# Kernel optimization log

Hardware: AMD Instinct MI355X
Metric: run time of the kernel (lower is better)

## Reference

```python
import jax, jax.numpy as jnp
import numpy as np

T, B = 32, 512          # frames, batch
HALF = 42               # rows per hand (21 landmarks x 2 coords)
HF = 300                # per-hand feature size
HID = 500               # hidden size
OUT = 10                # output classes
DN = ('NCH', 'OIH', 'NCH')


def setup_inputs() -> dict:
    key = jax.random.key(0)
    ks = jax.random.split(key, 18)
    n = lambda k, s: jax.random.normal(k, s, dtype=jnp.float32) * 0.05
    return dict(
        hand_data=jax.random.normal(ks[0], (T, B, 2 * HALF), dtype=jnp.float32),
        hidden=jnp.zeros((B, HID), jnp.float32),
        l_conv_w=n(ks[1], (16, 2, 2)), l_conv_b=n(ks[2], (16,)),
        l_fc_w=n(ks[3], (HF, 304)),    l_fc_b=n(ks[4], (HF,)),
        r_conv_w=n(ks[5], (16, 2, 2)), r_conv_b=n(ks[6], (16,)),
        r_fc_w=n(ks[7], (HF, 304)),    r_fc_b=n(ks[8], (HF,)),
        conv2_w=n(ks[9], (32, 2, 2)),  conv2_b=n(ks[10], (32,)),
        l2_w=n(ks[11], (HID, 9504)),   l2_b=n(ks[12], (HID,)),
        h2h_w=n(ks[13], (HID, HID)),   h2h_b=n(ks[14], (HID,)),
        out_w=n(ks[15], (OUT, HID)),   out_b=n(ks[16], (OUT,)),
    )


def _maxpool1d(y, k):
    return jax.lax.reduce_window(y, -jnp.inf, jax.lax.max,
                                 (1, 1, k), (1, 1, 1), 'VALID')


def _hand(x, cw, cb, fw, fb):
    # x: (N, 2, 21) -> conv k2 -> (N,16,20) -> relu -> pool k2 -> (N,16,19)
    y = jax.lax.conv_general_dilated(x, cw, (1,), 'VALID', dimension_numbers=DN)
    y = jax.nn.relu(y + cb[None, :, None])
    y = _maxpool1d(y, 2)
    y = y.reshape(y.shape[0], -1)          # (N, 304)
    return jax.nn.relu(y @ fw.T + fb)      # (N, 300)


def reference(hand_data, hidden,
              l_conv_w, l_conv_b, l_fc_w, l_fc_b,
              r_conv_w, r_conv_b, r_fc_w, r_fc_b,
              conv2_w, conv2_b, l2_w, l2_b,
              h2h_w, h2h_b, out_w, out_b):
    t, b, r = hand_data.shape
    half = r // 2
    # (T,B,42) -> (T*B,21,2) -> (T*B,2,21); per-frame branches have no
    # recurrence, so we vectorize them over all frames at once.
    left = jnp.swapaxes(hand_data[:, :, :half].reshape(t * b, -1, 2), 1, 2)
    right = jnp.swapaxes(hand_data[:, :, half:].reshape(t * b, -1, 2), 1, 2)
    lo = _hand(left, l_conv_w, l_conv_b, l_fc_w, l_fc_b)    # (T*B, 300)
    ro = _hand(right, r_conv_w, r_conv_b, r_fc_w, r_fc_b)   # (T*B, 300)
    both = jnp.stack([lo, ro], axis=1)                       # (T*B, 2, 300)
    y = jax.lax.conv_general_dilated(both, conv2_w, (1,), 'VALID',
                                     dimension_numbers=DN)   # (T*B, 32, 299)
    y = jax.nn.relu(y + conv2_b[None, :, None])
    y = _maxpool1d(y, 3)                                     # (T*B, 32, 297)
    y = y.reshape(t * b, -1)                                 # (T*B, 9504)
    i2h = (y @ l2_w.T + l2_b).reshape(t, b, -1)              # (T, B, 500)

    def step(h, i2h_t):
        h = h @ h2h_w.T + h2h_b                              # hidden = h2h(hidden)
        out = jax.nn.relu((i2h_t + h) @ out_w.T + out_b)
        return h, out

    hidden, outs = jax.lax.scan(step, hidden, i2h)
    return outs[-1], hidden
```

## Files before the change

### kernel.cpp

```cpp
#include <hip/hip_runtime.h>
#include <hip/hip_bf16.h>


typedef __attribute__((ext_vector_type(8))) unsigned short us8;
typedef __attribute__((ext_vector_type(8))) __bf16 bf8v;
typedef __attribute__((ext_vector_type(4))) float f4v;

static __device__ __forceinline__ unsigned short f2bf(float x) {
    __hip_bfloat16 h = __float2bfloat16(x);
    return *reinterpret_cast<unsigned short*>(&h);
}

static __device__ __forceinline__ void gload16(const void* g, void* s) {
    typedef __attribute__((address_space(1))) const void gv_t;
    typedef __attribute__((address_space(3))) void sv_t;
    __builtin_amdgcn_global_load_lds((gv_t*)g, (sv_t*)s, 16, 0, 0);
}

static __device__ __forceinline__ float4 ldg4_guard(
    const float* __restrict__ p, int r, int R, int c, int C, int ld)
{
    float4 v = make_float4(0.f, 0.f, 0.f, 0.f);
    if (r < R) {
        if (c + 3 < C) {
            v = *(const float4*)(p + (size_t)r * ld + c);
        } else {
            float tmp[4] = {0.f, 0.f, 0.f, 0.f};
            for (int u = 0; u < 4; ++u)
                if (c + u < C) tmp[u] = p[(size_t)r * ld + c + u];
            v = make_float4(tmp[0], tmp[1], tmp[2], tmp[3]);
        }
    }
    return v;
}

#define KSTR 9536

__global__ __launch_bounds__(256, 2) void mfma_bt(
    const unsigned short* __restrict__ A, const unsigned short* __restrict__ B,
    float* __restrict__ Cp, int nper, int ntot)
{
    __shared__ alignas(16) unsigned short Al[2][4096];
    __shared__ alignas(16) unsigned short Bl[2][4096];
    const int bm = blockIdx.x * 64, bn = blockIdx.y * 64;
    const int z = blockIdx.z;
    int s0 = z * nper;
    int s1 = s0 + nper; if (s1 > ntot) s1 = ntot;
    const int ns = s1 - s0;
    const int t = threadIdx.x, w = t >> 6, l = t & 63;
    const int srow = l >> 3;
    const int sslot = (l & 7) ^ srow;
    const int wm = (w >> 1) * 32, wn = (w & 1) * 32;
    const int fr = l & 15, jj = l >> 4;
    f4v acc[2][2] = {};

    const unsigned short* Ab = A + (size_t)(bm + 16 * w + srow) * KSTR + sslot * 8;
    const unsigned short* Bb = B + (size_t)(bn + 16 * w + srow) * KSTR + sslot * 8;

#define STAGE(buf, st)                                                          \
    {                                                                           \
        size_t k0 = (size_t)(s0 + (st)) * 64;                                   \
        _Pragma("unroll")                                                       \
        for (int q = 0; q < 2; ++q) {                                           \
            gload16(Ab + (size_t)(8 * q) * KSTR + k0,                           \
                    &Al[buf][(16 * w + 8 * q) * 64]);                           \
            gload16(Bb + (size_t)(8 * q) * KSTR + k0,                           \
                    &Bl[buf][(16 * w + 8 * q) * 64]);                           \
        }                                                                       \
    }

#define COMPUTE(buf)                                                            \
    {                                                                           \
        _Pragma("unroll")                                                       \
        for (int kk = 0; kk < 2; ++kk) {                                        \
            bf8v af[2], bf[2];                                                  \
            _Pragma("unroll")                                                   \
            for (int f = 0; f < 2; ++f) {                                       \
                int rA = wm + f * 16 + fr;                                      \
                int pA = (jj + 4 * kk) ^ (rA & 7);                              \
                af[f] = __builtin_bit_cast(bf8v,                                \
                        *(const us8*)&Al[buf][rA * 64 + pA * 8]);               \
                int rB = wn + f * 16 + fr;                                      \
                int pB = (jj + 4 * kk) ^ (rB & 7);                              \
                bf[f] = __builtin_bit_cast(bf8v,                                \
                        *(const us8*)&Bl[buf][rB * 64 + pB * 8]);               \
            }                                                                   \
            _Pragma("unroll")                                                   \
            for (int fi = 0; fi < 2; ++fi)                                      \
                _Pragma("unroll")                                               \
                for (int fj = 0; fj < 2; ++fj)                                  \
                    acc[fi][fj] = __builtin_amdgcn_mfma_f32_16x16x32_bf16(      \
                        af[fi], bf[fj], acc[fi][fj], 0, 0, 0);                  \
        }                                                                       \
    }

    STAGE(0, 0);
    __syncthreads();
    int cur = 0;
    for (int st = 0; st < ns; ++st) {
        if (st + 1 < ns) STAGE(cur ^ 1, st + 1);
        COMPUTE(cur);
        __syncthreads();
        cur ^= 1;
    }

    float* Cz = Cp + (size_t)z * 262144;
#pragma unroll
    for (int fi = 0; fi < 2; ++fi)
#pragma unroll
        for (int fj = 0; fj < 2; ++fj)
#pragma unroll
            for (int r = 0; r < 4; ++r) {
                int m = bm + wm + fi * 16 + jj * 4 + r;
                int n = bn + wn + fj * 16 + fr;
                Cz[(size_t)m * 512 + n] = acc[fi][fj][r];
            }
#undef STAGE
#undef COMPUTE
}


__global__ __launch_bounds__(256) void fc_gemm(
    const float* __restrict__ hpL, const float* __restrict__ hpR,
    const float* __restrict__ lfw, const float* __restrict__ rfw,
    const float* __restrict__ lfb, const float* __restrict__ rfb,
    float* __restrict__ both)
{
    __shared__ alignas(16) float As[16][68];
    __shared__ alignas(16) float Bs[16][68];
    const int hand = blockIdx.z;
    const float* A = hand ? hpR : hpL;
    const float* B = hand ? rfw : lfw;
    const float* bias = hand ? rfb : lfb;
    const int t = threadIdx.x;
    const int bm = blockIdx.x * 64, bn = blockIdx.y * 64;
    const int lr = t >> 2, kq = (t & 3) * 4;
    const int ty = t >> 4, tx = t & 15;
    float acc[4][4] = {};
    float4 a0 = *(const float4*)(A + (size_t)(bm + lr) * 304 + kq);
    float4 b0 = (bn + lr < 300)
        ? *(const float4*)(B + (size_t)(bn + lr) * 304 + kq)
        : make_float4(0.f, 0.f, 0.f, 0.f);
    for (int ks = 0; ks < 19; ++ks) {
        __syncthreads();
        As[kq + 0][lr] = a0.x; As[kq + 1][lr] = a0.y;
        As[kq + 2][lr] = a0.z; As[kq + 3][lr] = a0.w;
        Bs[kq + 0][lr] = b0.x; Bs[kq + 1][lr] = b0.y;
        Bs[kq + 2][lr] = b0.z; Bs[kq + 3][lr] = b0.w;
        __syncthreads();
        if (ks < 18) {
            int kb = (ks + 1) * 16 + kq;
            a0 = *(const float4*)(A + (size_t)(bm + lr) * 304 + kb);
            b0 = (bn + lr < 300)
                ? *(const float4*)(B + (size_t)(bn + lr) * 304 + kb)
                : make_float4(0.f, 0.f, 0.f, 0.f);
        }
#pragma unroll
        for (int k = 0; k < 16; ++k) {
            float4 av = *(const float4*)&As[k][ty * 4];
            float4 bv = *(const float4*)&Bs[k][tx * 4];
            float aa[4] = {av.x, av.y, av.z, av.w};
            float bb[4] = {bv.x, bv.y, bv.z, bv.w};
#pragma unroll
            for (int i = 0; i < 4; ++i)
#pragma unroll
                for (int j = 0; j < 4; ++j)
                    acc[i][j] = fmaf(aa[i], bb[j], acc[i][j]);
        }
    }
#pragma unroll
    for (int i = 0; i < 4; ++i) {
        int m = bm + ty * 4 + i;
#pragma unroll
        for (int j = 0; j < 4; ++j) {
            int n = bn + tx * 4 + j;
            if (n < 300)
                both[(size_t)m * 600 + hand * 300 + n] =
                    fmaxf(acc[i][j] + bias[n], 0.f);
        }
    }
}

__global__ __launch_bounds__(256) void sq_gemm(
    const float* __restrict__ P, float* __restrict__ Psum)
{
    __shared__ alignas(16) float As[16][68];
    __shared__ alignas(16) float Bs[16][68];
    const int t = threadIdx.x;
    const int bm = blockIdx.x * 64, bn = blockIdx.y * 64, z = blockIdx.z;
    const int k0 = z * 128;
    const int kend = (k0 + 128 < 500) ? k0 + 128 : 500;
    const int lr = t >> 2, kq = (t & 3) * 4;
    const int kr = t >> 4, cq = (t & 15) * 4;
    const int ty = t >> 4, tx = t & 15;
    float acc[4][4] = {};
    float4 a0 = ldg4_guard(P, bm + lr, 500, k0 + kq, kend, 500);
    float4 b0 = ldg4_guard(P, k0 + kr, kend, bn + cq, 500, 500);
    for (int ks = 0; ks < 8; ++ks) {
        __syncthreads();
        As[kq + 0][lr] = a0.x; As[kq + 1][lr] = a0.y;
        As[kq + 2][lr] = a0.z; As[kq + 3][lr] = a0.w;
        *(float4*)&Bs[kr][cq] = b0;
        __syncthreads();
        if (ks < 7) {
            a0 = ldg4_guard(P, bm + lr, 500, k0 + (ks + 1) * 16 + kq, kend, 500);
            b0 = ldg4_guard(P, k0 + (ks + 1) * 16 + kr, kend, bn + cq, 500, 500);
        }
#pragma unroll
        for (int k = 0; k < 16; ++k) {
            float4 av = *(const float4*)&As[k][ty * 4];
            float4 bv = *(const float4*)&Bs[k][tx * 4];
            float aa[4] = {av.x, av.y, av.z, av.w};
            float bb[4] = {bv.x, bv.y, bv.z, bv.w};
#pragma unroll
            for (int i = 0; i < 4; ++i)
#pragma unroll
                for (int j = 0; j < 4; ++j)
                    acc[i][j] = fmaf(aa[i], bb[j], acc[i][j]);
        }
    }
    float* Cz = Psum + (size_t)z * 250000;
#pragma unroll
    for (int i = 0; i < 4; ++i) {
        int m = bm + ty * 4 + i;
        if (m >= 500) continue;
#pragma unroll
        for (int j = 0; j < 4; ++j) {
            int n = bn + tx * 4 + j;
            if (n < 500) Cz[(size_t)m * 500 + n] = acc[i][j];
        }
    }
}

__global__ __launch_bounds__(256) void sq_red(
    const float* __restrict__ Psum, float* __restrict__ Pn,
    const float* __restrict__ u, const float* __restrict__ Pold,
    float* __restrict__ un)
{
    __shared__ float red[4];
    const int x = blockIdx.x, t = threadIdx.x;
    if (x < 977) {
        int idx = x * 256 + t;
        if (idx < 250000)
            Pn[idx] = Psum[idx] + Psum[250000 + idx] +
                      Psum[500000 + idx] + Psum[750000 + idx];
    } else {
        int j = x - 977;
        const float* row = Pold + (size_t)j * 500;
        float s = 0.f;
        for (int a = t; a < 500; a += 256) s += u[a] * row[a];
        for (int off = 32; off; off >>= 1) s += __shfl_down(s, off);
        if ((t & 63) == 0) red[t >> 6] = s;
        __syncthreads();
        if (t == 0) un[j] = red[0] + red[1] + red[2] + red[3] + u[j];
    }
}

__global__ __launch_bounds__(256) void h_gemm(
    const float* __restrict__ A, const float* __restrict__ B,
    float* __restrict__ Hsum)
{
    __shared__ alignas(16) float As[16][68];
    __shared__ alignas(16) float Bs[16][68];
    const int t = threadIdx.x;
    const int bm = blockIdx.x * 64, bn = blockIdx.y * 64, z = blockIdx.z;
    const int k0 = z * 128;
    const int kend = (k0 + 128 < 500) ? k0 + 128 : 500;
    const int lr = t >> 2, kq = (t & 3) * 4;
    const int ty = t >> 4, tx = t & 15;
    float acc[4][4] = {};
    float4 a0 = ldg4_guard(A, bm + lr, 512, k0 + kq, kend, 500);
    float4 b0 = ldg4_guard(B, bn + lr, 500, k0 + kq, kend, 500);
    for (int ks = 0; ks < 8; ++ks) {
        __syncthreads();
        As[kq + 0][lr] = a0.x; As[kq + 1][lr] = a0.y;
        As[kq + 2][lr] = a0.z; As[kq + 3][lr] = a0.w;
        Bs[kq + 0][lr] = b0.x; Bs[kq + 1][lr] = b0.y;
        Bs[kq + 2][lr] = b0.z; Bs[kq + 3][lr] = b0.w;
        __syncthreads();
        if (ks < 7) {
            a0 = ldg4_guard(A, bm + lr, 512, k0 + (ks + 1) * 16 + kq, kend, 500);
            b0 = ldg4_guard(B, bn + lr, 500, k0 + (ks + 1) * 16 + kq, kend, 500);
        }
#pragma unroll
        for (int k = 0; k < 16; ++k) {
            float4 av = *(const float4*)&As[k][ty * 4];
            float4 bv = *(const float4*)&Bs[k][tx * 4];
            float aa[4] = {av.x, av.y, av.z, av.w};
            float bb[4] = {bv.x, bv.y, bv.z, bv.w};
#pragma unroll
            for (int i = 0; i < 4; ++i)
#pragma unroll
                for (int j = 0; j < 4; ++j)
                    acc[i][j] = fmaf(aa[i], bb[j], acc[i][j]);
        }
    }
    float* Cz = Hsum + (size_t)z * 256000;
#pragma unroll
    for (int i = 0; i < 4; ++i) {
        int m = bm + ty * 4 + i;
#pragma unroll
        for (int j = 0; j < 4; ++j) {
            int n = bn + tx * 4 + j;
            if (n < 500) Cz[(size_t)m * 500 + n] = acc[i][j];
        }
    }
}

__global__ __launch_bounds__(128) void hand_conv(
    const float* __restrict__ hand,
    const float* __restrict__ lcw, const float* __restrict__ lcb,
    const float* __restrict__ rcw, const float* __restrict__ rcb,
    float* __restrict__ hpL, float* __restrict__ hpR)
{
    const int b = blockIdx.x;
    __shared__ float x[84];
    __shared__ float cw[2][64];
    __shared__ float cb[2][16];
    const int t = threadIdx.x;
    if (t < 84) x[t] = hand[(size_t)b * 84 + t];
    if (t < 64) { cw[0][t] = lcw[t]; cw[1][t] = rcw[t]; }
    if (t < 16) { cb[0][t] = lcb[t]; cb[1][t] = rcb[t]; }
    __syncthreads();
    for (int idx = t; idx < 608; idx += 128) {
        int hi = idx / 304, rem = idx % 304;
        int o = rem / 19, p = rem % 19;
        int off = hi * 42;
        const float* w = cw[hi];
        float w00 = w[o * 4], w01 = w[o * 4 + 1], w10 = w[o * 4 + 2], w11 = w[o * 4 + 3];
        float bs = cb[hi][o];
        float c0 = w00 * x[off + 2 * p] + w01 * x[off + 2 * p + 2] +
                   w10 * x[off + 2 * p + 1] + w11 * x[off + 2 * p + 3] + bs;
        float c1 = w00 * x[off + 2 * p + 2] + w01 * x[off + 2 * p + 4] +
                   w10 * x[off + 2 * p + 3] + w11 * x[off + 2 * p + 5] + bs;
        float v = fmaxf(fmaxf(c0, c1), 0.f);
        (hi ? hpR : hpL)[(size_t)b * 304 + rem] = v;
    }
}

__global__ __launch_bounds__(256) void conv2_feat(
    const float* __restrict__ both, const float* __restrict__ w2g,
    const float* __restrict__ b2g, unsigned short* __restrict__ feat)
{
    const int b = blockIdx.x, t = threadIdx.x;
    __shared__ float s[600];
    __shared__ float w2[128];
    __shared__ float b2[32];
    for (int i = t; i < 600; i += 256) s[i] = both[(size_t)b * 600 + i];
    if (t < 128) w2[t] = w2g[t];
    if (t < 32) b2[t] = b2g[t];
    __syncthreads();
    for (int idx = t; idx < 9536; idx += 256) {
        unsigned short ov = 0;
        if (idx < 9504) {
            int o = idx / 297, p = idx - o * 297;
            float w0 = w2[o * 4], w1 = w2[o * 4 + 1];
            float w2v = w2[o * 4 + 2], w3 = w2[o * 4 + 3], bb = b2[o];
            float m = -1e30f;
#pragma unroll
            for (int q = 0; q < 3; ++q) {
                float c = w0 * s[p + q] + w1 * s[p + q + 1] +
                          w2v * s[300 + p + q] + w3 * s[301 + p + q] + bb;
                m = fmaxf(m, c);
            }
            ov = f2bf(fmaxf(m, 0.f));
        }
        feat[(size_t)b * 9536 + idx] = ov;
    }
}

__global__ __launch_bounds__(256) void cvt_w(
    const float* __restrict__ W, unsigned short* __restrict__ Wb)
{
    int idx = blockIdx.x * 256 + threadIdx.x;
    int row = idx / 1192;
    int k8 = (idx - row * 1192) * 8;
    if (row >= 512) return;
    us8 o = (us8)0;
    if (row < 500 && k8 < 9504) {
        const float* p = W + (size_t)row * 9504 + k8;
        float4 v0 = *(const float4*)p;
        float4 v1 = *(const float4*)(p + 4);
        o[0] = f2bf(v0.x); o[1] = f2bf(v0.y); o[2] = f2bf(v0.z); o[3] = f2bf(v0.w);
        o[4] = f2bf(v1.x); o[5] = f2bf(v1.y); o[6] = f2bf(v1.z); o[7] = f2bf(v1.w);
    }
    *(us8*)(Wb + (size_t)row * 9536 + k8) = o;
}

__global__ __launch_bounds__(256) void out_final(
    const float* __restrict__ Cp, const float* __restrict__ l2b,
    const float* __restrict__ Hsum, const float* __restrict__ u32,
    const float* __restrict__ ow, const float* __restrict__ ob,
    float* __restrict__ out, float* __restrict__ hout)
{
    const int b = blockIdx.x, t = threadIdx.x;
    __shared__ float sj[512];
    __shared__ float red[10][4];
    for (int j = t; j < 500; j += 256) {
        float ih = l2b[j];
#pragma unroll
        for (int zz = 0; zz < 8; ++zz)
            ih += Cp[(size_t)zz * 262144 + (size_t)b * 512 + j];
        float h = u32[j];
#pragma unroll
        for (int zz = 0; zz < 4; ++zz)
            h += Hsum[(size_t)zz * 256000 + (size_t)b * 500 + j];
        hout[(size_t)b * 500 + j] = h;
        sj[j] = ih + h;
    }
    __syncthreads();
    const int w = t >> 6;
    for (int o = 0; o < 10; ++o) {
        float acc = 0.f;
        if (t < 500) acc += sj[t] * ow[o * 500 + t];
        if (t + 256 < 500) acc += sj[t + 256] * ow[o * 500 + t + 256];
        for (int off = 32; off; off >>= 1) acc += __shfl_down(acc, off);
        if ((t & 63) == 0) red[o][w] = acc;
    }
    __syncthreads();
    if (t < 10)
        out[(size_t)b * 10 + t] =
            fmaxf(red[t][0] + red[t][1] + red[t][2] + red[t][3] + ob[t], 0.f);
}

extern "C" void kernel_launch(void* const* d_in, const int* in_sizes, int n_in,
                              void* d_out, int out_size, void* d_ws, size_t ws_size,
                              hipStream_t stream) {
    const float* hand   = (const float*)d_in[0];
    const float* hidden = (const float*)d_in[1];
    const float* lcw = (const float*)d_in[2];
    const float* lcb = (const float*)d_in[3];
    const float* lfw = (const float*)d_in[4];
    const float* lfb = (const float*)d_in[5];
    const float* rcw = (const float*)d_in[6];
    const float* rcb = (const float*)d_in[7];
    const float* rfw = (const float*)d_in[8];
    const float* rfb = (const float*)d_in[9];
    const float* w2  = (const float*)d_in[10];
    const float* b2  = (const float*)d_in[11];
    const float* l2w = (const float*)d_in[12];
    const float* l2b = (const float*)d_in[13];
    const float* hw  = (const float*)d_in[14];
    const float* hb  = (const float*)d_in[15];
    const float* ow  = (const float*)d_in[16];
    const float* ob  = (const float*)d_in[17];

    char* wsb = (char*)d_ws;
    float* Cp   = (float*)wsb;
    float* hpL  = (float*)wsb;
    float* hpR  = (float*)(wsb + 622592);
    float* both = (float*)(wsb + 1245184);
    char* base1 = wsb + 8388608;
    unsigned short* featb = (unsigned short*)base1;
    unsigned short* wbf   = (unsigned short*)(base1 + 9764864);
    float* Psum = (float*)base1;
    float* Pa   = (float*)(base1 + 4000000);
    float* Pb   = (float*)(base1 + 5000000);
    float* ua   = (float*)(base1 + 6000000);
    float* ub   = (float*)(base1 + 6002000);
    float* Hsum = (float*)(base1 + 9764864);

    float* out  = (float*)d_out;
    float* hout = out + 5120;

    cvt_w<<<2384, 256, 0, stream>>>(l2w, wbf);
    hand_conv<<<512, 128, 0, stream>>>(hand + (size_t)31 * 512 * 84,
                                       lcw, lcb, rcw, rcb, hpL, hpR);
    fc_gemm<<<dim3(8, 5, 2), 256, 0, stream>>>(hpL, hpR, lfw, rfw, lfb, rfb, both);
    conv2_feat<<<512, 256, 0, stream>>>(both, w2, b2, featb);
    mfma_bt<<<dim3(8, 8, 8), 256, 0, stream>>>(featb, wbf, Cp, 19, 149);

    const float* Pcur = hw;
    const float* ucur = hb;
    float* Pn[5] = {Pa, Pb, Pa, Pb, Pa};
    float* un[5] = {ua, ub, ua, ub, ua};
    for (int i = 0; i < 5; i++) {
        sq_gemm<<<dim3(8, 8, 4), 256, 0, stream>>>(Pcur, Psum);
        sq_red<<<1477, 256, 0, stream>>>(Psum, Pn[i], ucur, Pcur, un[i]);
        Pcur = Pn[i];
        ucur = un[i];
    }
    h_gemm<<<dim3(8, 8, 4), 256, 0, stream>>>(hidden, Pcur, Hsum);
    out_final<<<512, 256, 0, stream>>>(Cp, l2b, Hsum, ucur, ow, ob, out, hout);
}
```

Before: 149.6 us.

## Fuse split-K partial reduction into repeated-squaring GEMM loads, drop reduce kernels

Removes the separate sq_red reduction kernels. Each squaring level now sums the four split-K partial products while loading its operands, and the same launch also computes the bias-vector update. This halves the number of launches in the recurrence chain and avoids writing and re-reading the reduced matrix. In exchange, every operand tile load now reads four source buffers, so redundant global reads grow. The change also flattens grid indexing, raises mfma_bt's minimum-blocks-per-CU launch bound from 2 to 4, and changes h_gemm to a 2-way K split.

```diff
diff --git a/kernel.cpp b/kernel.cpp
--- a/kernel.cpp
+++ b/kernel.cpp
@@ -34,18 +34,29 @@
     return v;
 }
 
+static __device__ __forceinline__ float4 ldg4_sum(
+    const float* __restrict__ p, int nsrc, int r, int R, int c, int C, int ld)
+{
+    float4 v = ldg4_guard(p, r, R, c, C, ld);
+    for (int s = 1; s < nsrc; ++s) {
+        float4 w = ldg4_guard(p + (size_t)s * 250000, r, R, c, C, ld);
+        v.x += w.x; v.y += w.y; v.z += w.z; v.w += w.w;
+    }
+    return v;
+}
+
 #define KSTR 9536
 
-__global__ __launch_bounds__(256, 2) void mfma_bt(
+__global__ __launch_bounds__(256, 4) void mfma_bt(
     const unsigned short* __restrict__ A, const unsigned short* __restrict__ B,
-    float* __restrict__ Cp, int nper, int ntot)
+    float* __restrict__ Cp)
 {
     __shared__ alignas(16) unsigned short Al[2][4096];
     __shared__ alignas(16) unsigned short Bl[2][4096];
-    const int bm = blockIdx.x * 64, bn = blockIdx.y * 64;
-    const int z = blockIdx.z;
-    int s0 = z * nper;
-    int s1 = s0 + nper; if (s1 > ntot) s1 = ntot;
+    const int lid = blockIdx.x;
+    const int z = lid & 7;
+    const int bm = ((lid >> 3) & 7) * 64, bn = ((lid >> 6) & 7) * 64;
+    int s0 = z * 19, s1 = s0 + 19; if (s1 > 149) s1 = 149;
     const int ns = s1 - s0;
     const int t = threadIdx.x, w = t >> 6, l = t & 63;
     const int srow = l >> 3;
@@ -54,21 +65,18 @@
     const int fr = l & 15, jj = l >> 4;
     f4v acc[2][2] = {};
 
-    const unsigned short* Ab = A + (size_t)(bm + 16 * w + srow) * KSTR + sslot * 8;
-    const unsigned short* Bb = B + (size_t)(bn + 16 * w + srow) * KSTR + sslot * 8;
+    const unsigned short* Ab = A + (size_t)(bm + 16*w + srow) * KSTR + sslot * 8;
+    const unsigned short* Bb = B + (size_t)(bn + 16*w + srow) * KSTR + sslot * 8;
 
 #define STAGE(buf, st)                                                          \
     {                                                                           \
         size_t k0 = (size_t)(s0 + (st)) * 64;                                   \
         _Pragma("unroll")                                                       \
         for (int q = 0; q < 2; ++q) {                                           \
-            gload16(Ab + (size_t)(8 * q) * KSTR + k0,                           \
-                    &Al[buf][(16 * w + 8 * q) * 64]);                           \
-            gload16(Bb + (size_t)(8 * q) * KSTR + k0,                           \
-                    &Bl[buf][(16 * w + 8 * q) * 64]);                           \
+            gload16(Ab + (size_t)(8*q) * KSTR + k0, &Al[buf][(16*w + 8*q)*64]); \
+            gload16(Bb + (size_t)(8*q) * KSTR + k0, &Bl[buf][(16*w + 8*q)*64]); \
         }                                                                       \
     }
-
 #define COMPUTE(buf)                                                            \
     {                                                                           \
         _Pragma("unroll")                                                       \
@@ -77,11 +85,11 @@
             _Pragma("unroll")                                                   \
             for (int f = 0; f < 2; ++f) {                                       \
                 int rA = wm + f * 16 + fr;                                      \
-                int pA = (jj + 4 * kk) ^ (rA & 7);                              \
+                int pA = (jj + 4*kk) ^ (rA & 7);                                \
                 af[f] = __builtin_bit_cast(bf8v,                                \
                         *(const us8*)&Al[buf][rA * 64 + pA * 8]);               \
                 int rB = wn + f * 16 + fr;                                      \
-                int pB = (jj + 4 * kk) ^ (rB & 7);                              \
+                int pB = (jj + 4*kk) ^ (rB & 7);                                \
                 bf[f] = __builtin_bit_cast(bf8v,                                \
                         *(const us8*)&Bl[buf][rB * 64 + pB * 8]);               \
             }                                                                   \
@@ -103,7 +111,6 @@
         __syncthreads();
         cur ^= 1;
     }
-
     float* Cz = Cp + (size_t)z * 262144;
 #pragma unroll
     for (int fi = 0; fi < 2; ++fi)
@@ -119,6 +126,124 @@
 #undef COMPUTE
 }
 
+__global__ __launch_bounds__(256) void sq_level(
+    const float* __restrict__ src, int nsrc, float* __restrict__ dst,
+    const float* __restrict__ u_in, float* __restrict__ u_out)
+{
+    __shared__ alignas(16) float As[16][68];
+    __shared__ alignas(16) float Bs[16][68];
+    const int lid = blockIdx.x, t = threadIdx.x;
+    if (lid >= 256) {
+        const int j = lid - 256;
+        float* red = (float*)As;
+        float s = 0.f;
+        for (int a = t; a < 500; a += 256) {
+            float p = src[(size_t)j * 500 + a];
+            for (int q = 1; q < nsrc; ++q)
+                p += src[(size_t)q * 250000 + (size_t)j * 500 + a];
+            s += u_in[a] * p;
+        }
+        for (int off = 32; off; off >>= 1) s += __shfl_down(s, off);
+        if ((t & 63) == 0) red[t >> 6] = s;
+        __syncthreads();
+        if (t == 0) u_out[j] = red[0] + red[1] + red[2] + red[3] + u_in[j];
+        return;
+    }
+    const int z = lid & 3;
+    const int bm = ((lid >> 2) & 7) * 64, bn = (lid >> 5) * 64;
+    const int k0 = z * 125, kend = k0 + 125;
+    const int lr = t >> 2, kq = (t & 3) * 4;
+    const int kr = t >> 4, cq = (t & 15) * 4;
+    const int ty = t >> 4, tx = t & 15;
+    float acc[4][4] = {};
+    float4 a0 = ldg4_sum(src, nsrc, bm + lr, 500, k0 + kq, kend, 500);
+    float4 b0 = ldg4_sum(src, nsrc, k0 + kr, kend, bn + cq, 500, 500);
+    for (int ks = 0; ks < 8; ++ks) {
+        __syncthreads();
+        As[kq+0][lr] = a0.x; As[kq+1][lr] = a0.y;
+        As[kq+2][lr] = a0.z; As[kq+3][lr] = a0.w;
+        *(float4*)&Bs[kr][cq] = b0;
+        __syncthreads();
+        if (ks < 7) {
+            a0 = ldg4_sum(src, nsrc, bm + lr, 500, k0 + (ks+1)*16 + kq, kend, 500);
+            b0 = ldg4_sum(src, nsrc, k0 + (ks+1)*16 + kr, kend, bn + cq, 500, 500);
+        }
+#pragma unroll
+        for (int k = 0; k < 16; ++k) {
+            float4 av = *(const float4*)&As[k][ty * 4];
+            float4 bv = *(const float4*)&Bs[k][tx * 4];
+            float aa[4] = {av.x, av.y, av.z, av.w};
+            float bb[4] = {bv.x, bv.y, bv.z, bv.w};
+#pragma unroll
+            for (int i = 0; i < 4; ++i)
+#pragma unroll
+                for (int j = 0; j < 4; ++j)
+                    acc[i][j] = fmaf(aa[i], bb[j], acc[i][j]);
+        }
+    }
+    float* Cz = dst + (size_t)z * 250000;
+#pragma unroll
+    for (int i = 0; i < 4; ++i) {
+        int m = bm + ty * 4 + i;
+        if (m >= 500) continue;
+#pragma unroll
+        for (int j = 0; j < 4; ++j) {
+            int n = bn + tx * 4 + j;
+            if (n < 500) Cz[(size_t)m * 500 + n] = acc[i][j];
+        }
+    }
+}
+
+__global__ __launch_bounds__(256) void h_gemm(
+    const float* __restrict__ A, const float* __restrict__ src,
+    float* __restrict__ Hsum)
+{
+    __shared__ alignas(16) float As[16][68];
+    __shared__ alignas(16) float Bs[16][68];
+    const int rid = blockIdx.x, t = threadIdx.x;
+    const int z = rid & 1;
+    const int bm = ((rid >> 1) & 7) * 64, bn = ((rid >> 4) & 7) * 64;
+    const int k0 = z * 250, kend = k0 + 250;
+    const int lr = t >> 2, kq = (t & 3) * 4;
+    const int ty = t >> 4, tx = t & 15;
+    float acc[4][4] = {};
+    float4 a0 = ldg4_guard(A, bm + lr, 512, k0 + kq, kend, 500);
+    float4 b0 = ldg4_sum(src, 4, bn + lr, 500, k0 + kq, kend, 500);
+    for (int ks = 0; ks < 16; ++ks) {
+        __syncthreads();
+        As[kq+0][lr] = a0.x; As[kq+1][lr] = a0.y;
+        As[kq+2][lr] = a0.z; As[kq+3][lr] = a0.w;
+        Bs[kq+0][lr] = b0.x; Bs[kq+1][lr] = b0.y;
+        Bs[kq+2][lr] = b0.z; Bs[kq+3][lr] = b0.w;
+        __syncthreads();
+        if (ks < 15) {
+            a0 = ldg4_guard(A, bm + lr, 512, k0 + (ks+1)*16 + kq, kend, 500);
+            b0 = ldg4_sum(src, 4, bn + lr, 500, k0 + (ks+1)*16 + kq, kend, 500);
+        }
+#pragma unroll
+        for (int k = 0; k < 16; ++k) {
+            float4 av = *(const float4*)&As[k][ty * 4];
+            float4 bv = *(const float4*)&Bs[k][tx * 4];
+            float aa[4] = {av.x, av.y, av.z, av.w};
+            float bb[4] = {bv.x, bv.y, bv.z, bv.w};
+#pragma unroll
+            for (int i = 0; i < 4; ++i)
+#pragma unroll
+                for (int j = 0; j < 4; ++j)
+                    acc[i][j] = fmaf(aa[i], bb[j], acc[i][j]);
+        }
+    }
+    float* Cz = Hsum + (size_t)z * 256000;
+#pragma unroll
+    for (int i = 0; i < 4; ++i) {
+        int m = bm + ty * 4 + i;
+#pragma unroll
+        for (int j = 0; j < 4; ++j) {
+            int n = bn + tx * 4 + j;
+            if (n < 500) Cz[(size_t)m * 500 + n] = acc[i][j];
+        }
+    }
+}
 
 __global__ __launch_bounds__(256) void fc_gemm(
     const float* __restrict__ hpL, const float* __restrict__ hpR,
@@ -143,10 +268,10 @@
         : make_float4(0.f, 0.f, 0.f, 0.f);
     for (int ks = 0; ks < 19; ++ks) {
         __syncthreads();
-        As[kq + 0][lr] = a0.x; As[kq + 1][lr] = a0.y;
-        As[kq + 2][lr] = a0.z; As[kq + 3][lr] = a0.w;
-        Bs[kq + 0][lr] = b0.x; Bs[kq + 1][lr] = b0.y;
-        Bs[kq + 2][lr] = b0.z; Bs[kq + 3][lr] = b0.w;
+        As[kq+0][lr] = a0.x; As[kq+1][lr] = a0.y;
+        As[kq+2][lr] = a0.z; As[kq+3][lr] = a0.w;
+        Bs[kq+0][lr] = b0.x; Bs[kq+1][lr] = b0.y;
+        Bs[kq+2][lr] = b0.z; Bs[kq+3][lr] = b0.w;
         __syncthreads();
         if (ks < 18) {
             int kb = (ks + 1) * 16 + kq;
@@ -177,132 +302,6 @@
             if (n < 300)
                 both[(size_t)m * 600 + hand * 300 + n] =
                     fmaxf(acc[i][j] + bias[n], 0.f);
-        }
-    }
-}
-
-__global__ __launch_bounds__(256) void sq_gemm(
-    const float* __restrict__ P, float* __restrict__ Psum)
-{
-    __shared__ alignas(16) float As[16][68];
-    __shared__ alignas(16) float Bs[16][68];
-    const int t = threadIdx.x;
-    const int bm = blockIdx.x * 64, bn = blockIdx.y * 64, z = blockIdx.z;
-    const int k0 = z * 128;
-    const int kend = (k0 + 128 < 500) ? k0 + 128 : 500;
-    const int lr = t >> 2, kq = (t & 3) * 4;
-    const int kr = t >> 4, cq = (t & 15) * 4;
-    const int ty = t >> 4, tx = t & 15;
-    float acc[4][4] = {};
-    float4 a0 = ldg4_guard(P, bm + lr, 500, k0 + kq, kend, 500);
-    float4 b0 = ldg4_guard(P, k0 + kr, kend, bn + cq, 500, 500);
-    for (int ks = 0; ks < 8; ++ks) {
-        __syncthreads();
-        As[kq + 0][lr] = a0.x; As[kq + 1][lr] = a0.y;
-        As[kq + 2][lr] = a0.z; As[kq + 3][lr] = a0.w;
-        *(float4*)&Bs[kr][cq] = b0;
-        __syncthreads();
-        if (ks < 7) {
-            a0 = ldg4_guard(P, bm + lr, 500, k0 + (ks + 1) * 16 + kq, kend, 500);
-            b0 = ldg4_guard(P, k0 + (ks + 1) * 16 + kr, kend, bn + cq, 500, 500);
-        }
-#pragma unroll
-        for (int k = 0; k < 16; ++k) {
-            float4 av = *(const float4*)&As[k][ty * 4];
-            float4 bv = *(const float4*)&Bs[k][tx * 4];
-            float aa[4] = {av.x, av.y, av.z, av.w};
-            float bb[4] = {bv.x, bv.y, bv.z, bv.w};
-#pragma unroll
-            for (int i = 0; i < 4; ++i)
-#pragma unroll
-                for (int j = 0; j < 4; ++j)
-                    acc[i][j] = fmaf(aa[i], bb[j], acc[i][j]);
-        }
-    }
-    float* Cz = Psum + (size_t)z * 250000;
-#pragma unroll
-    for (int i = 0; i < 4; ++i) {
-        int m = bm + ty * 4 + i;
-        if (m >= 500) continue;
-#pragma unroll
-        for (int j = 0; j < 4; ++j) {
-            int n = bn + tx * 4 + j;
-            if (n < 500) Cz[(size_t)m * 500 + n] = acc[i][j];
-        }
-    }
-}
-
-__global__ __launch_bounds__(256) void sq_red(
-    const float* __restrict__ Psum, float* __restrict__ Pn,
-    const float* __restrict__ u, const float* __restrict__ Pold,
-    float* __restrict__ un)
-{
-    __shared__ float red[4];
-    const int x = blockIdx.x, t = threadIdx.x;
-    if (x < 977) {
-        int idx = x * 256 + t;
-        if (idx < 250000)
-            Pn[idx] = Psum[idx] + Psum[250000 + idx] +
-                      Psum[500000 + idx] + Psum[750000 + idx];
-    } else {
-        int j = x - 977;
-        const float* row = Pold + (size_t)j * 500;
-        float s = 0.f;
-        for (int a = t; a < 500; a += 256) s += u[a] * row[a];
-        for (int off = 32; off; off >>= 1) s += __shfl_down(s, off);
-        if ((t & 63) == 0) red[t >> 6] = s;
-        __syncthreads();
-        if (t == 0) un[j] = red[0] + red[1] + red[2] + red[3] + u[j];
-    }
-}
-
-__global__ __launch_bounds__(256) void h_gemm(
-    const float* __restrict__ A, const float* __restrict__ B,
-    float* __restrict__ Hsum)
-{
-    __shared__ alignas(16) float As[16][68];
-    __shared__ alignas(16) float Bs[16][68];
-    const int t = threadIdx.x;
-    const int bm = blockIdx.x * 64, bn = blockIdx.y * 64, z = blockIdx.z;
-    const int k0 = z * 128;
-    const int kend = (k0 + 128 < 500) ? k0 + 128 : 500;
-    const int lr = t >> 2, kq = (t & 3) * 4;
-    const int ty = t >> 4, tx = t & 15;
-    float acc[4][4] = {};
-    float4 a0 = ldg4_guard(A, bm + lr, 512, k0 + kq, kend, 500);
-    float4 b0 = ldg4_guard(B, bn + lr, 500, k0 + kq, kend, 500);
-    for (int ks = 0; ks < 8; ++ks) {
-        __syncthreads();
-        As[kq + 0][lr] = a0.x; As[kq + 1][lr] = a0.y;
-        As[kq + 2][lr] = a0.z; As[kq + 3][lr] = a0.w;
-        Bs[kq + 0][lr] = b0.x; Bs[kq + 1][lr] = b0.y;
-        Bs[kq + 2][lr] = b0.z; Bs[kq + 3][lr] = b0.w;
-        __syncthreads();
-        if (ks < 7) {
-            a0 = ldg4_guard(A, bm + lr, 512, k0 + (ks + 1) * 16 + kq, kend, 500);
-            b0 = ldg4_guard(B, bn + lr, 500, k0 + (ks + 1) * 16 + kq, kend, 500);
-        }
-#pragma unroll
-        for (int k = 0; k < 16; ++k) {
-            float4 av = *(const float4*)&As[k][ty * 4];
-            float4 bv = *(const float4*)&Bs[k][tx * 4];
-            float aa[4] = {av.x, av.y, av.z, av.w};
-            float bb[4] = {bv.x, bv.y, bv.z, bv.w};
-#pragma unroll
-            for (int i = 0; i < 4; ++i)
-#pragma unroll
-                for (int j = 0; j < 4; ++j)
-                    acc[i][j] = fmaf(aa[i], bb[j], acc[i][j]);
-        }
-    }
-    float* Cz = Hsum + (size_t)z * 256000;
-#pragma unroll
-    for (int i = 0; i < 4; ++i) {
-        int m = bm + ty * 4 + i;
-#pragma unroll
-        for (int j = 0; j < 4; ++j) {
-            int n = bn + tx * 4 + j;
-            if (n < 500) Cz[(size_t)m * 500 + n] = acc[i][j];
         }
     }
 }
@@ -327,12 +326,12 @@
         int o = rem / 19, p = rem % 19;
         int off = hi * 42;
         const float* w = cw[hi];
-        float w00 = w[o * 4], w01 = w[o * 4 + 1], w10 = w[o * 4 + 2], w11 = w[o * 4 + 3];
+        float w00 = w[o*4], w01 = w[o*4+1], w10 = w[o*4+2], w11 = w[o*4+3];
         float bs = cb[hi][o];
-        float c0 = w00 * x[off + 2 * p] + w01 * x[off + 2 * p + 2] +
-                   w10 * x[off + 2 * p + 1] + w11 * x[off + 2 * p + 3] + bs;
-        float c1 = w00 * x[off + 2 * p + 2] + w01 * x[off + 2 * p + 4] +
-                   w10 * x[off + 2 * p + 3] + w11 * x[off + 2 * p + 5] + bs;
+        float c0 = w00*x[off+2*p]   + w01*x[off+2*p+2] +
+                   w10*x[off+2*p+1] + w11*x[off+2*p+3] + bs;
+        float c1 = w00*x[off+2*p+2] + w01*x[off+2*p+4] +
+                   w10*x[off+2*p+3] + w11*x[off+2*p+5] + bs;
         float v = fmaxf(fmaxf(c0, c1), 0.f);
         (hi ? hpR : hpL)[(size_t)b * 304 + rem] = v;
     }
@@ -354,13 +353,12 @@
         unsigned short ov = 0;
         if (idx < 9504) {
             int o = idx / 297, p = idx - o * 297;
-            float w0 = w2[o * 4], w1 = w2[o * 4 + 1];
-            float w2v = w2[o * 4 + 2], w3 = w2[o * 4 + 3], bb = b2[o];
+            float w0 = w2[o*4], w1 = w2[o*4+1], wv = w2[o*4+2], w3 = w2[o*4+3];
+            float bb = b2[o];
             float m = -1e30f;
 #pragma unroll
             for (int q = 0; q < 3; ++q) {
-                float c = w0 * s[p + q] + w1 * s[p + q + 1] +
-                          w2v * s[300 + p + q] + w3 * s[301 + p + q] + bb;
+                float c = w0*s[p+q] + w1*s[p+q+1] + wv*s[300+p+q] + w3*s[301+p+q] + bb;
                 m = fmaxf(m, c);
             }
             ov = f2bf(fmaxf(m, 0.f));
@@ -401,10 +399,8 @@
 #pragma unroll
         for (int zz = 0; zz < 8; ++zz)
             ih += Cp[(size_t)zz * 262144 + (size_t)b * 512 + j];
-        float h = u32[j];
-#pragma unroll
-        for (int zz = 0; zz < 4; ++zz)
-            h += Hsum[(size_t)zz * 256000 + (size_t)b * 500 + j];
+        float h = u32[j] + Hsum[(size_t)b * 500 + j] +
+                  Hsum[256000 + (size_t)b * 500 + j];
         hout[(size_t)b * 500 + j] = h;
         sj[j] = ih + h;
     }
@@ -447,39 +443,37 @@
 
     char* wsb = (char*)d_ws;
     float* Cp   = (float*)wsb;
-    float* hpL  = (float*)wsb;
-    float* hpR  = (float*)(wsb + 622592);
-    float* both = (float*)(wsb + 1245184);
-    char* base1 = wsb + 8388608;
-    unsigned short* featb = (unsigned short*)base1;
-    unsigned short* wbf   = (unsigned short*)(base1 + 9764864);
-    float* Psum = (float*)base1;
-    float* Pa   = (float*)(base1 + 4000000);
-    float* Pb   = (float*)(base1 + 5000000);
-    float* ua   = (float*)(base1 + 6000000);
-    float* ub   = (float*)(base1 + 6002000);
-    float* Hsum = (float*)(base1 + 9764864);
+    unsigned short* featb = (unsigned short*)(wsb + 8388608);
+    unsigned short* wbf   = (unsigned short*)(wsb + 18153472);
+    float* Q    = (float*)(wsb + 27918336);
+    float* R    = (float*)(wsb + 31918336);
+    float* u1   = (float*)(wsb + 35918336);
+    float* u2   = u1 + 512;
+    float* u3   = u2 + 512;
+    float* u4   = u3 + 512;
+    float* u5   = u4 + 512;
+    float* hpL  = (float*)(wsb + 35928576);
+    float* hpR  = (float*)(wsb + 36551168);
+    float* both = (float*)(wsb + 37173760);
+    float* Hsum = (float*)(wsb + 38402560);
 
     float* out  = (float*)d_out;
     float* hout = out + 5120;
 
+    const float* hand31 = hand + (size_t)31 * 512 * 84;
+
     cvt_w<<<2384, 256, 0, stream>>>(l2w, wbf);
-    hand_conv<<<512, 128, 0, stream>>>(hand + (size_t)31 * 512 * 84,
-                                       lcw, lcb, rcw, rcb, hpL, hpR);
+    hand_conv<<<512, 128, 0, stream>>>(hand31, lcw, lcb, rcw, rcb, hpL, hpR);
     fc_gemm<<<dim3(8, 5, 2), 256, 0, stream>>>(hpL, hpR, lfw, rfw, lfb, rfb, both);
     conv2_feat<<<512, 256, 0, stream>>>(both, w2, b2, featb);
-    mfma_bt<<<dim3(8, 8, 8), 256, 0, stream>>>(featb, wbf, Cp, 19, 149);
-
-    const float* Pcur = hw;
-    const float* ucur = hb;
-    float* Pn[5] = {Pa, Pb, Pa, Pb, Pa};
-    float* un[5] = {ua, ub, ua, ub, ua};
-    for (int i = 0; i < 5; i++) {
-        sq_gemm<<<dim3(8, 8, 4), 256, 0, stream>>>(Pcur, Psum);
-        sq_red<<<1477, 256, 0, stream>>>(Psum, Pn[i], ucur, Pcur, un[i]);
-        Pcur = Pn[i];
-        ucur = un[i];
-    }
-    h_gemm<<<dim3(8, 8, 4), 256, 0, stream>>>(hidden, Pcur, Hsum);
-    out_final<<<512, 256, 0, stream>>>(Cp, l2b, Hsum, ucur, ow, ob, out, hout);
-}
+    mfma_bt<<<512, 256, 0, stream>>>(featb, wbf, Cp);
+
+    sq_level<<<756, 256, 0, stream>>>(hw, 1, Q, hb, u1);
+    sq_level<<<756, 256, 0, stream>>>(Q, 4, R, u1, u2);
+    sq_level<<<756, 256, 0, stream>>>(R, 4, Q, u2, u3);
+    sq_level<<<756, 256, 0, stream>>>(Q, 4, R, u3, u4);
+    sq_level<<<756, 256, 0, stream>>>(R, 4, Q, u4, u5);
+
+    h_gemm<<<128, 256, 0, stream>>>(hidden, Q, Hsum);
+    out_final<<<512, 256, 0, stream>>>(Cp, l2b, Hsum, u5, ow, ob, out, hout);
+}
```

Result: slower. 207.6 us (+38.8%).
